# Kernel tuning notes

Hardware: AMD Instinct MI355X
Metric: run time of the kernel (lower is better)

## Reference

```python
import jax, jax.numpy as jnp
import numpy as np

NUM_USER = 24000
NUM_ITEM = 8000
DIM_E = 64
V_DIM = 2048
T_DIM = 384
TOPK = 10
N_UI_LAYERS = 2
LAMBDA = 0.9
N_INTER = 400000


def _build_sim(x):
    xn = x / jnp.linalg.norm(x, axis=-1, keepdims=True)
    return xn @ xn.T


def _knn_sym(sim, topk):
    # top-k per row -> sparse graph with symmetric (D^-1/2 A D^-1/2) normalization
    n = sim.shape[0]
    val, ind = jax.lax.top_k(sim, topk)            # [n, k]
    row = jnp.repeat(jnp.arange(n), topk)
    w = val.reshape(-1)
    col = ind.reshape(-1)
    deg = jax.ops.segment_sum(w, row, num_segments=n)
    dis = jnp.where(deg > 0, deg ** -0.5, 0.0)     # inf -> 0 as in torch masked_fill
    return col, dis[row] * w * dis[col]


def setup_inputs() -> dict:
    key = jax.random.key(0)
    ks = jax.random.split(key, 12)
    user_emb = jax.random.normal(ks[0], (NUM_USER, DIM_E), jnp.float32) * 0.1
    item_emb = jax.random.normal(ks[1], (NUM_ITEM, DIM_E), jnp.float32) * 0.1
    v_feat = jax.random.normal(ks[2], (NUM_ITEM, V_DIM), jnp.float32)
    t_feat = jax.random.normal(ks[3], (NUM_ITEM, T_DIM), jnp.float32)
    W_v = jax.random.normal(ks[4], (V_DIM, DIM_E), jnp.float32) * (1.0 / np.sqrt(V_DIM))
    b_v = jnp.zeros((DIM_E,), jnp.float32)
    W_t = jax.random.normal(ks[5], (T_DIM, DIM_E), jnp.float32) * (1.0 / np.sqrt(T_DIM))
    b_t = jnp.zeros((DIM_E,), jnp.float32)
    Wq1 = jax.random.normal(ks[6], (DIM_E, DIM_E), jnp.float32) * (1.0 / np.sqrt(DIM_E))
    bq1 = jnp.zeros((DIM_E,), jnp.float32)
    wq2 = jax.random.normal(ks[7], (DIM_E,), jnp.float32) * (1.0 / np.sqrt(DIM_E))
    # bipartite user-item interaction edges, symmetrized (as in __init__)
    u = jax.random.randint(ks[8], (N_INTER,), 0, NUM_USER)
    it = jax.random.randint(ks[9], (N_INTER,), 0, NUM_ITEM) + NUM_USER
    ei = jnp.stack([u, it])
    edge_index = jnp.concatenate([ei, ei[::-1]], axis=1)  # [2, 2*N_INTER]
    # original (frozen) multimodal KNN graphs built from raw features at init
    orig_img_cols, orig_img_w = _knn_sym(_build_sim(v_feat), TOPK)
    orig_txt_cols, orig_txt_w = _knn_sym(_build_sim(t_feat), TOPK)
    return {"user_emb": user_emb, "item_emb": item_emb, "v_feat": v_feat,
            "t_feat": t_feat, "W_v": W_v, "b_v": b_v, "W_t": W_t, "b_t": b_t,
            "Wq1": Wq1, "bq1": bq1, "wq2": wq2,
            "orig_img_w": orig_img_w, "orig_txt_w": orig_txt_w,
            "edge_index": edge_index,
            "orig_img_cols": orig_img_cols, "orig_txt_cols": orig_txt_cols}


def reference(user_emb, item_emb, v_feat, t_feat, W_v, b_v, W_t, b_t,
              Wq1, bq1, wq2, orig_img_w, orig_txt_w,
              edge_index, orig_img_cols, orig_txt_cols):
    n_user, n_item = user_emb.shape[0], item_emb.shape[0]
    # modality projections
    image_feats = v_feat @ W_v + b_v
    text_feats = t_feat @ W_t + b_t
    # fresh KNN graphs from projected features (build_item_graph=True path)
    img_cols, img_w = _knn_sym(_build_sim(image_feats), TOPK)
    txt_cols, txt_w = _knn_sym(_build_sim(text_feats), TOPK)
    row = jnp.repeat(jnp.arange(n_item), TOPK)

    def fused_spmm(cols_new, w_new, cols_orig, w_orig, x):
        # (1-lam)*A_new + lam*A_orig, applied as a single sparse matmul
        rows = jnp.concatenate([row, row])
        cols = jnp.concatenate([cols_new, cols_orig])
        w = jnp.concatenate([(1.0 - LAMBDA) * w_new,
                             LAMBDA * jax.lax.stop_gradient(w_orig)])
        return jax.ops.segment_sum(w[:, None] * x[cols], rows, num_segments=n_item)

    # NOTE: source bug reproduced - mm_layers loop always re-reads item_embedding,
    # so effective propagation depth is 1 regardless of mm_layers.
    image_item = fused_spmm(img_cols, img_w, orig_img_cols, orig_img_w, item_emb)
    text_item = fused_spmm(txt_cols, txt_w, orig_txt_cols, orig_txt_w, item_emb)

    def q(x):
        return jnp.tanh(x @ Wq1 + bq1) @ wq2  # [n_item]

    att = jnp.stack([q(image_item), q(text_item)], axis=-1)  # [n_item, 2]
    wgt = jax.nn.softmax(att, axis=-1)
    h = wgt[:, :1] * image_item + wgt[:, 1:] * text_item

    # user-item GCN propagation with sym degree normalization
    ego = jnp.concatenate([user_emb, item_emb], axis=0)
    n = ego.shape[0]
    r, c = edge_index[0], edge_index[1]
    deg = jax.ops.segment_sum(jnp.ones_like(r, dtype=ego.dtype), r, num_segments=n)
    dis = jnp.where(deg > 0, deg ** -0.5, 0.0)
    norm = dis[r] * dis[c]
    embs = [ego]
    for _ in range(N_UI_LAYERS):
        ego = jax.ops.segment_sum(norm[:, None] * ego[c], r, num_segments=n)
        embs.append(ego)
    all_emb = jnp.mean(jnp.stack(embs, axis=1), axis=1)
    u_g, i_g = all_emb[:n_user], all_emb[n_user:]
    h_norm = h / jnp.maximum(jnp.linalg.norm(h, axis=1, keepdims=True), 1e-12)
    i_g = i_g + h_norm
    return jnp.concatenate([u_g, i_g], axis=0)
```

## Files before the change

kernel.cpp:

```cpp
#include <hip/hip_runtime.h>
#include <math.h>

#define N_USER 24000
#define N_ITEM 8000
#define N_NODE 32000
#define N_EDGE 800000
#define NJC    16
#define JCH    512

typedef __attribute__((ext_vector_type(8))) short bf16x8;
typedef __attribute__((ext_vector_type(4))) float f32x4;

__device__ __forceinline__ float wred_sum(float v) {
#pragma unroll
  for (int off = 32; off; off >>= 1) v += __shfl_xor(v, off, 64);
  return v;
}

__device__ __forceinline__ unsigned short f2bf(float f) {
  unsigned int u = __float_as_uint(f);
  unsigned int r = (u + 0x7fffu + ((u >> 16) & 1u)) >> 16;
  return (unsigned short)r;
}
__device__ __forceinline__ float bf2f(unsigned short h) {
  return __uint_as_float(((unsigned int)h) << 16);
}

__device__ __forceinline__ unsigned int umx(unsigned int a, unsigned int b) { return a > b ? a : b; }
__device__ __forceinline__ unsigned int umn(unsigned int a, unsigned int b) { return a < b ? a : b; }

__device__ __forceinline__ float key_val(unsigned int k) {
  return ((float)(int)(k >> 13) - 131080.0f) * (1.0f / 131072.0f);
}
__device__ __forceinline__ int key_idx(unsigned int k) {
  return 8191 - (int)(k & 8191u);
}

__global__ __launch_bounds__(256) void gemm_dual(
    const float* __restrict__ Xi, const float* __restrict__ Wi,
    const float* __restrict__ Xt, const float* __restrict__ Wt,
    float* __restrict__ Pi, float* __restrict__ Pt)
{
  __shared__ float As[32 * 64];
  __shared__ float Bs[32 * 64];
  const int tid = threadIdx.x;
  const int m0 = blockIdx.x * 64;
  const int cy = blockIdx.y;
  const float* X; const float* W; float* out; int K, kc0, Klen;
  if (cy < 8) { X = Xi; W = Wi; K = 2048; Klen = 256; kc0 = cy * 256;
                out = Pi + (size_t)cy * N_ITEM * 64; }
  else        { X = Xt; W = Wt; K = 384;  Klen = 128; kc0 = (cy - 8) * 128;
                out = Pt + (size_t)(cy - 8) * N_ITEM * 64; }
  const int tr = tid >> 4, tc = tid & 15;
  float acc[4][4] = {};
  for (int k0 = kc0; k0 < kc0 + Klen; k0 += 32) {
    __syncthreads();
#pragma unroll
    for (int l = 0; l < 2; ++l) {
      int f4 = tid + l * 256;
      int r = f4 >> 3, kq = f4 & 7;
      float4 a = *(const float4*)(X + (size_t)(m0 + r) * K + k0 + kq * 4);
      As[(kq * 4 + 0) * 64 + r] = a.x;
      As[(kq * 4 + 1) * 64 + r] = a.y;
      As[(kq * 4 + 2) * 64 + r] = a.z;
      As[(kq * 4 + 3) * 64 + r] = a.w;
      int kb = f4 >> 4, nq = f4 & 15;
      *(float4*)(Bs + kb * 64 + nq * 4) =
          *(const float4*)(W + (size_t)(k0 + kb) * 64 + nq * 4);
    }
    __syncthreads();
#pragma unroll
    for (int k = 0; k < 32; ++k) {
      float4 a4 = *(const float4*)(As + k * 64 + tr * 4);
      float4 b4 = *(const float4*)(Bs + k * 64 + tc * 4);
      float av[4] = {a4.x, a4.y, a4.z, a4.w};
      float bv[4] = {b4.x, b4.y, b4.z, b4.w};
#pragma unroll
      for (int ri = 0; ri < 4; ++ri)
#pragma unroll
        for (int ci = 0; ci < 4; ++ci) acc[ri][ci] += av[ri] * bv[ci];
    }
  }
#pragma unroll
  for (int ri = 0; ri < 4; ++ri) {
    float4 o;
    o.x = acc[ri][0]; o.y = acc[ri][1]; o.z = acc[ri][2]; o.w = acc[ri][3];
    *(float4*)(out + (size_t)(m0 + tr * 4 + ri) * 64 + tc * 4) = o;
  }
}

__global__ __launch_bounds__(256) void norm_dual(
    const float* __restrict__ Pi, const float* __restrict__ bi,
    unsigned short* __restrict__ Xhi, unsigned short* __restrict__ Xli,
    const float* __restrict__ Pt, const float* __restrict__ bt,
    unsigned short* __restrict__ Xht, unsigned short* __restrict__ Xlt)
{
  const float* P; const float* bias; unsigned short *Xh, *Xl; int nk;
  if (blockIdx.y == 0) { P = Pi; bias = bi; Xh = Xhi; Xl = Xli; nk = 8; }
  else                 { P = Pt; bias = bt; Xh = Xht; Xl = Xlt; nk = 3; }
  int row = blockIdx.x * 4 + (threadIdx.x >> 6);
  int lane = threadIdx.x & 63;
  size_t o = (size_t)row * 64 + lane;
  float v = bias[lane];
  for (int q = 0; q < nk; ++q) v += P[(size_t)q * N_ITEM * 64 + o];
  float ss = wred_sum(v * v);
  float xn = v * rsqrtf(ss);
  unsigned short hi = f2bf(xn);
  Xh[o] = hi;
  Xl[o] = f2bf(xn - bf2f(hi));
}

__global__ __launch_bounds__(256) void sim_topk_mfma(
    const unsigned short* __restrict__ Xhi, const unsigned short* __restrict__ Xli,
    const unsigned short* __restrict__ Xht, const unsigned short* __restrict__ Xlt,
    unsigned int* __restrict__ pk)
{
  __shared__ char lds[2 * 2 * 32 * 128];
  const unsigned short* Xh = blockIdx.z ? Xht : Xhi;
  const unsigned short* Xl = blockIdx.z ? Xlt : Xli;
  unsigned int* pkm = pk + (size_t)blockIdx.z * N_ITEM * (NJC * 10);

  const int tid = threadIdx.x;
  const int l = tid & 63;
  const int wid = tid >> 6;
  const int ib = blockIdx.x * 128 + wid * 32;
  const int jc = blockIdx.y * JCH;

  bf16x8 bh[2][2], bl[2][2];
#pragma unroll
  for (int s = 0; s < 2; ++s) {
    int irow = ib + s * 16 + (l & 15);
    if (irow > N_ITEM - 1) irow = N_ITEM - 1;
    int ksl = (l >> 4) * 8;
#pragma unroll
    for (int kh = 0; kh < 2; ++kh) {
      bh[s][kh] = *(const bf16x8*)(Xh + (size_t)irow * 64 + kh * 32 + ksl);
      bl[s][kh] = *(const bf16x8*)(Xl + (size_t)irow * 64 + kh * 32 + ksl);
    }
  }

  unsigned int K0[10], K1[10];
#pragma unroll
  for (int t = 0; t < 10; ++t) { K0[t] = 0u; K1[t] = 0u; }

  auto stage = [&](int b, int p) {
    int row = tid >> 3, cb = (tid & 7) * 16;
    int gr = jc + p * 32 + row;
    if (gr > N_ITEM - 1) gr = N_ITEM - 1;
    int4 vh = *(const int4*)(Xh + (size_t)gr * 64 + (cb >> 1));
    int4 vl = *(const int4*)(Xl + (size_t)gr * 64 + (cb >> 1));
    int bo = (row * 128 + cb) ^ ((row & 7) << 4);
    *(int4*)(lds + b * 8192 + bo) = vh;
    *(int4*)(lds + b * 8192 + 4096 + bo) = vl;
  };

  stage(0, 0);
  int cur = 0;
  for (int p = 0; p < 16; ++p) {
    __syncthreads();
    if (p < 15) stage(cur ^ 1, p + 1);
    const char* ldsH = lds + cur * 8192;
    const char* ldsL = ldsH + 4096;
    f32x4 acc[2][2] = {};
#pragma unroll
    for (int t = 0; t < 2; ++t) {
      int jr = t * 16 + (l & 15);
      int sw = (jr & 7) << 4;
      int rb = jr * 128 + ((l >> 4) << 4);
      bf16x8 ah0 = *(const bf16x8*)(ldsH + (rb ^ sw));
      bf16x8 ah1 = *(const bf16x8*)(ldsH + ((rb + 64) ^ sw));
      bf16x8 al0 = *(const bf16x8*)(ldsL + (rb ^ sw));
      bf16x8 al1 = *(const bf16x8*)(ldsL + ((rb + 64) ^ sw));
#pragma unroll
      for (int s = 0; s < 2; ++s) {
        acc[t][s] = __builtin_amdgcn_mfma_f32_16x16x32_bf16(ah0, bh[s][0], acc[t][s], 0, 0, 0);
        acc[t][s] = __builtin_amdgcn_mfma_f32_16x16x32_bf16(ah1, bh[s][1], acc[t][s], 0, 0, 0);
        acc[t][s] = __builtin_amdgcn_mfma_f32_16x16x32_bf16(ah0, bl[s][0], acc[t][s], 0, 0, 0);
        acc[t][s] = __builtin_amdgcn_mfma_f32_16x16x32_bf16(ah1, bl[s][1], acc[t][s], 0, 0, 0);
        acc[t][s] = __builtin_amdgcn_mfma_f32_16x16x32_bf16(al0, bh[s][0], acc[t][s], 0, 0, 0);
        acc[t][s] = __builtin_amdgcn_mfma_f32_16x16x32_bf16(al1, bh[s][1], acc[t][s], 0, 0, 0);
      }
    }
    const int jg0 = jc + p * 32 + ((l >> 4) << 2);
#pragma unroll
    for (int s = 0; s < 2; ++s) {
      unsigned int* K = s ? K1 : K0;
#pragma unroll
      for (int t = 0; t < 2; ++t) {
#pragma unroll
        for (int r = 0; r < 4; ++r) {
          int jj = jg0 + t * 16 + r;
          float f = acc[t][s][r];
          unsigned int v19 = (unsigned int)(int)(f * 131072.0f + 131080.0f);
          unsigned int key = (v19 << 13) | (unsigned int)(8191 - jj);
          key = (jj < N_ITEM) ? key : 0u;
#pragma unroll
          for (int q = 0; q < 10; ++q) {
            unsigned int mn = umn(K[q], key);
            K[q] = umx(K[q], key);
            key = mn;
          }
        }
      }
    }
    cur ^= 1;
  }

#pragma unroll
  for (int s = 0; s < 2; ++s) {
    unsigned int* K = s ? K1 : K0;
    unsigned int kv[10];
#pragma unroll
    for (int t = 0; t < 10; ++t) {
      unsigned int m = K[0];
      m = umx(m, (unsigned int)__shfl_xor((int)m, 16, 64));
      m = umx(m, (unsigned int)__shfl_xor((int)m, 32, 64));
      bool own = (K[0] == m);
#pragma unroll
      for (int q2 = 0; q2 < 9; ++q2) K[q2] = own ? K[q2 + 1] : K[q2];
      K[9] = own ? 0u : K[9];
      kv[t] = m;
    }
    int i = ib + s * 16 + (l & 15);
    if (l < 16 && i < N_ITEM) {
      size_t base = ((size_t)i * NJC + blockIdx.y) * 10;
#pragma unroll
      for (int t = 0; t < 10; ++t) pkm[base + t] = kv[t];
    }
  }
}

__global__ __launch_bounds__(256) void merge_topk(
    const unsigned int* __restrict__ pk,
    float* __restrict__ tv_i, int* __restrict__ tc_i, float* __restrict__ dis_i,
    float* __restrict__ tv_t, int* __restrict__ tc_t, float* __restrict__ dis_t)
{
  float* tv; int* tc; float* dis;
  if (blockIdx.y == 0) { tv = tv_i; tc = tc_i; dis = dis_i; }
  else                 { tv = tv_t; tc = tc_t; dis = dis_t; }
  int lane = threadIdx.x & 63;
  int row = blockIdx.x * 4 + (threadIdx.x >> 6);
  size_t base = (size_t)blockIdx.y * N_ITEM * (NJC * 10) + (size_t)row * (NJC * 10);
  unsigned int k0 = pk[base + lane];
  unsigned int k1 = pk[base + 64 + lane];
  unsigned int k2 = (lane < 32) ? pk[base + 128 + lane] : 0u;
  float deg = 0.f, keepv = 0.f; int keepc = 0;
  for (int t = 0; t < 10; ++t) {
    unsigned int m = umx(umx(k0, k1), k2);
#pragma unroll
    for (int off = 32; off; off >>= 1)
      m = umx(m, (unsigned int)__shfl_xor((int)m, off, 64));
    deg += key_val(m);
    if (k0 == m) k0 = 0u;
    else if (k1 == m) k1 = 0u;
    else if (k2 == m) k2 = 0u;
    if (lane == t) { keepv = key_val(m); keepc = key_idx(m); }
  }
  if (lane < 10) { tv[(size_t)row * 10 + lane] = keepv; tc[(size_t)row * 10 + lane] = keepc; }
  if (lane == 0) dis[row] = deg > 0.f ? rsqrtf(deg) : 0.f;
}

__global__ __launch_bounds__(256) void spmm_attn(
    const float* __restrict__ tv_i, const int* __restrict__ tc_i, const float* __restrict__ dis_i,
    const float* __restrict__ ow_i, const int* __restrict__ oc_i,
    const float* __restrict__ tv_t, const int* __restrict__ tc_t, const float* __restrict__ dis_t,
    const float* __restrict__ ow_t, const int* __restrict__ oc_t,
    const float* __restrict__ item_emb,
    const float* __restrict__ Wq1, const float* __restrict__ bq1,
    const float* __restrict__ wq2, float* __restrict__ hn)
{
  __shared__ float Wlds[64 * 64];
  __shared__ float sm[4][2][64];
  int tid = threadIdx.x;
  int lane = tid & 63, wid = tid >> 6;
  int row = blockIdx.x * 4 + wid;
#pragma unroll
  for (int s = 0; s < 4; ++s) {
    int idx = tid + s * 256;
    ((float4*)Wlds)[idx] = ((const float4*)Wq1)[idx];
  }
  float a0 = 0.f, a1 = 0.f;
  {
    float disr = dis_i[row];
#pragma unroll
    for (int t = 0; t < 10; ++t) {
      int c = tc_i[(size_t)row * 10 + t];
      a0 += 0.1f * disr * tv_i[(size_t)row * 10 + t] * dis_i[c] * item_emb[(size_t)c * 64 + lane];
    }
#pragma unroll
    for (int t = 0; t < 10; ++t) {
      int c = oc_i[(size_t)row * 10 + t];
      a0 += 0.9f * ow_i[(size_t)row * 10 + t] * item_emb[(size_t)c * 64 + lane];
    }
  }
  {
    float disr = dis_t[row];
#pragma unroll
    for (int t = 0; t < 10; ++t) {
      int c = tc_t[(size_t)row * 10 + t];
      a1 += 0.1f * disr * tv_t[(size_t)row * 10 + t] * dis_t[c] * item_emb[(size_t)c * 64 + lane];
    }
#pragma unroll
    for (int t = 0; t < 10; ++t) {
      int c = oc_t[(size_t)row * 10 + t];
      a1 += 0.9f * ow_t[(size_t)row * 10 + t] * item_emb[(size_t)c * 64 + lane];
    }
  }
  sm[wid][0][lane] = a0;
  sm[wid][1][lane] = a1;
  __syncthreads();
  float y0 = bq1[lane], y1 = bq1[lane];
  for (int k = 0; k < 64; ++k) {
    float w = Wlds[k * 64 + lane];
    y0 += sm[wid][0][k] * w;
    y1 += sm[wid][1][k] * w;
  }
  float wq = wq2[lane];
  float s0 = wred_sum(tanhf(y0) * wq);
  float s1 = wred_sum(tanhf(y1) * wq);
  float mx = fmaxf(s0, s1);
  float e0 = expf(s0 - mx), e1 = expf(s1 - mx);
  float inv = 1.f / (e0 + e1);
  float h = (e0 * inv) * a0 + (e1 * inv) * a1;
  float n2 = wred_sum(h * h);
  float nrm = fmaxf(sqrtf(n2), 1e-12f);
  hn[(size_t)row * 64 + lane] = h / nrm;
}

__global__ void ui_zero(int* degi, int* cursor)
{
  int n = blockIdx.x * 256 + threadIdx.x;
  if (n < N_NODE) { degi[n] = 0; cursor[n] = 0; }
}

__global__ void ui_count(const int* __restrict__ r, int* degi)
{
  int e = blockIdx.x * 256 + threadIdx.x;
  if (e < N_EDGE) atomicAdd(&degi[r[e]], 1);
}

__global__ __launch_bounds__(256) void ui_blocksum(const int* __restrict__ degi, int* __restrict__ bsum)
{
  __shared__ int ws4[4];
  int tid = threadIdx.x;
  int v = degi[blockIdx.x * 256 + tid];
#pragma unroll
  for (int off = 32; off; off >>= 1) v += __shfl_xor(v, off, 64);
  if ((tid & 63) == 0) ws4[tid >> 6] = v;
  __syncthreads();
  if (tid == 0) bsum[blockIdx.x] = ws4[0] + ws4[1] + ws4[2] + ws4[3];
}

__global__ __launch_bounds__(128) void ui_scanb(const int* __restrict__ bsum, int* __restrict__ bbase, int* __restrict__ offs)
{
  __shared__ int s[128];
  int t = threadIdx.x;
  int v = (t < 125) ? bsum[t] : 0;
  s[t] = v;
  __syncthreads();
  for (int off = 1; off < 128; off <<= 1) {
    int tmp = (t >= off) ? s[t - off] : 0;
    __syncthreads();
    s[t] += tmp;
    __syncthreads();
  }
  if (t < 125) bbase[t] = s[t] - v;
  if (t == 127) offs[N_NODE] = s[127];
}

__global__ __launch_bounds__(256) void ui_scanc(const int* __restrict__ degi, const int* __restrict__ bbase,
                                                int* __restrict__ offs, float* __restrict__ disui)
{
  __shared__ int wt[4];
  int tid = threadIdx.x;
  int i = blockIdx.x * 256 + tid;
  int d = degi[i];
  int v = d;
#pragma unroll
  for (int off = 1; off < 64; off <<= 1) {
    int n = __shfl_up(v, off, 64);
    if ((tid & 63) >= off) v += n;
  }
  if ((tid & 63) == 63) wt[tid >> 6] = v;
  __syncthreads();
  int add = bbase[blockIdx.x];
  for (int w = 0; w < (tid >> 6); ++w) add += wt[w];
  offs[i] = add + v - d;
  disui[i] = d > 0 ? rsqrtf((float)d) : 0.f;
}

__global__ void ui_fill(const int* __restrict__ r, const int* __restrict__ c,
                        const int* __restrict__ offs, int* cursor, int* __restrict__ csr)
{
  int e = blockIdx.x * 256 + threadIdx.x;
  if (e < N_EDGE) {
    int rr = r[e];
    int pos = offs[rr] + atomicAdd(&cursor[rr], 1);
    csr[pos] = c[e];
  }
}

template <bool FIRST, bool FINAL>
__global__ __launch_bounds__(256) void ui_prop(
    const float* __restrict__ in, const float* __restrict__ ue,
    const float* __restrict__ ie, float* __restrict__ out,
    const int* __restrict__ offs, const int* __restrict__ csr,
    const float* __restrict__ dis, const float* __restrict__ hn)
{
  int tid = threadIdx.x;
  int lane = tid & 63, wid = tid >> 6;
  int row = blockIdx.x * 4 + wid;
  int q = lane >> 4, c4 = lane & 15;
  float4 acc = make_float4(0.f, 0.f, 0.f, 0.f);
  int e0 = offs[row], e1 = offs[row + 1];
  for (int e = e0 + q; e < e1; e += 4) {
    int cc = csr[e];
    const float* src = FIRST
        ? (cc < N_USER ? ue + (size_t)cc * 64 : ie + (size_t)(cc - N_USER) * 64)
        : in + (size_t)cc * 64;
    float4 v = *(const float4*)(src + c4 * 4);
    float d = dis[cc];
    acc.x += d * v.x; acc.y += d * v.y; acc.z += d * v.z; acc.w += d * v.w;
  }
#pragma unroll
  for (int off = 16; off <= 32; off <<= 1) {
    acc.x += __shfl_xor(acc.x, off, 64);
    acc.y += __shfl_xor(acc.y, off, 64);
    acc.z += __shfl_xor(acc.z, off, 64);
    acc.w += __shfl_xor(acc.w, off, 64);
  }
  if (q == 0) {
    float dr = dis[row];
    acc.x *= dr; acc.y *= dr; acc.z *= dr; acc.w *= dr;
    if (!FINAL) {
      *(float4*)(out + (size_t)row * 64 + c4 * 4) = acc;
    } else {
      float4 ego = (row < N_USER)
          ? *(const float4*)(ue + (size_t)row * 64 + c4 * 4)
          : *(const float4*)(ie + (size_t)(row - N_USER) * 64 + c4 * 4);
      float4 l1 = *(const float4*)(in + (size_t)row * 64 + c4 * 4);
      float4 o;
      o.x = (ego.x + l1.x + acc.x) * (1.f / 3.f);
      o.y = (ego.y + l1.y + acc.y) * (1.f / 3.f);
      o.z = (ego.z + l1.z + acc.z) * (1.f / 3.f);
      o.w = (ego.w + l1.w + acc.w) * (1.f / 3.f);
      if (row >= N_USER) {
        float4 h = *(const float4*)(hn + (size_t)(row - N_USER) * 64 + c4 * 4);
        o.x += h.x; o.y += h.y; o.z += h.z; o.w += h.w;
      }
      *(float4*)(out + (size_t)row * 64 + c4 * 4) = o;
    }
  }
}

extern "C" void kernel_launch(void* const* d_in, const int* in_sizes, int n_in,
                              void* d_out, int out_size, void* d_ws, size_t ws_size,
                              hipStream_t stream)
{
  (void)in_sizes; (void)n_in; (void)out_size; (void)ws_size;
  const float* user_emb = (const float*)d_in[0];
  const float* item_emb = (const float*)d_in[1];
  const float* v_feat   = (const float*)d_in[2];
  const float* t_feat   = (const float*)d_in[3];
  const float* W_v      = (const float*)d_in[4];
  const float* b_v      = (const float*)d_in[5];
  const float* W_t      = (const float*)d_in[6];
  const float* b_t      = (const float*)d_in[7];
  const float* Wq1      = (const float*)d_in[8];
  const float* bq1      = (const float*)d_in[9];
  const float* wq2      = (const float*)d_in[10];
  const float* ow_i     = (const float*)d_in[11];
  const float* ow_t     = (const float*)d_in[12];
  const int*   eidx     = (const int*)d_in[13];
  const int*   oc_i     = (const int*)d_in[14];
  const int*   oc_t     = (const int*)d_in[15];
  float* out = (float*)d_out;

  char* wp = (char*)d_ws;
  auto alloc = [&](size_t bytes) -> void* {
    void* p = (void*)wp;
    wp += (bytes + 255) & ~(size_t)255;
    return p;
  };
  char* regionA = (char*)alloc((size_t)8 * N_ITEM * 64 * 4 + 1024);
  char* regionB = (char*)alloc((size_t)N_NODE * 64 * 4 + 1024);
  float* Pp_i = (float*)regionA;
  float* Pp_t = (float*)regionB;
  unsigned int* pk = (unsigned int*)regionA;
  float* E1 = (float*)regionB;

  unsigned short* Xhi = (unsigned short*)alloc((size_t)N_ITEM * 64 * 2);
  unsigned short* Xli = (unsigned short*)alloc((size_t)N_ITEM * 64 * 2);
  unsigned short* Xht = (unsigned short*)alloc((size_t)N_ITEM * 64 * 2);
  unsigned short* Xlt = (unsigned short*)alloc((size_t)N_ITEM * 64 * 2);
  float* tv_i  = (float*)alloc((size_t)N_ITEM * 10 * 4);
  int*   tc_i  = (int*)  alloc((size_t)N_ITEM * 10 * 4);
  float* dis_i = (float*)alloc((size_t)N_ITEM * 4);
  float* tv_t  = (float*)alloc((size_t)N_ITEM * 10 * 4);
  int*   tc_t  = (int*)  alloc((size_t)N_ITEM * 10 * 4);
  float* dis_t = (float*)alloc((size_t)N_ITEM * 4);
  float* hn    = (float*)alloc((size_t)N_ITEM * 64 * 4);
  int*   degi  = (int*)  alloc((size_t)N_NODE * 4);
  int*   curs  = (int*)  alloc((size_t)N_NODE * 4);
  int*   offs  = (int*)  alloc((size_t)(N_NODE + 1) * 4);
  float* disui = (float*)alloc((size_t)N_NODE * 4);
  int*   csr   = (int*)  alloc((size_t)N_EDGE * 4);
  int*   bsum  = (int*)  alloc((size_t)128 * 4);
  int*   bbase = (int*)  alloc((size_t)128 * 4);

  gemm_dual<<<dim3(125, 11), 256, 0, stream>>>(v_feat, W_v, t_feat, W_t, Pp_i, Pp_t);
  norm_dual<<<dim3(2000, 2), 256, 0, stream>>>(Pp_i, b_v, Xhi, Xli, Pp_t, b_t, Xht, Xlt);
  sim_topk_mfma<<<dim3(63, NJC, 2), 256, 0, stream>>>(Xhi, Xli, Xht, Xlt, pk);
  merge_topk<<<dim3(2000, 2), 256, 0, stream>>>(pk, tv_i, tc_i, dis_i, tv_t, tc_t, dis_t);
  spmm_attn<<<2000, 256, 0, stream>>>(tv_i, tc_i, dis_i, ow_i, oc_i,
                                      tv_t, tc_t, dis_t, ow_t, oc_t,
                                      item_emb, Wq1, bq1, wq2, hn);
  ui_zero<<<125, 256, 0, stream>>>(degi, curs);
  ui_count<<<N_EDGE / 256, 256, 0, stream>>>(eidx, degi);
  ui_blocksum<<<125, 256, 0, stream>>>(degi, bsum);
  ui_scanb<<<1, 128, 0, stream>>>(bsum, bbase, offs);
  ui_scanc<<<125, 256, 0, stream>>>(degi, bbase, offs, disui);
  ui_fill<<<N_EDGE / 256, 256, 0, stream>>>(eidx, eidx + N_EDGE, offs, curs, csr);
  ui_prop<true, false><<<8000, 256, 0, stream>>>(nullptr, user_emb, item_emb, E1, offs, csr, disui, nullptr);
  ui_prop<false, true><<<8000, 256, 0, stream>>>(E1, user_emb, item_emb, out, offs, csr, disui, hn);
}
```

Before: 320.0 us.

## Enlarge GEMM row tile, specialize top-k epilogue masking, widen SpMM lanes

The projection GEMM now computes a 128-row tile per block, giving each thread 8x4 outputs, and pads the A tile stride in LDS. This halves the block count and clamps out-of-range rows. The similarity top-k epilogue precomputes the inverted column indices and applies the out-of-range mask only in the last column chunk. The UI propagation kernel has each lane handle 8 floats per edge and processes 8 edges in parallel per row, with one extra shuffle stage. These are separate local tweaks meant to raise arithmetic intensity and cut per-element overhead, at the cost of higher register use and fewer GEMM blocks.

```diff
diff --git a/kernel.cpp b/kernel.cpp
--- a/kernel.cpp
+++ b/kernel.cpp
@@ -36,15 +36,16 @@
   return 8191 - (int)(k & 8191u);
 }
 
+#define ASTR 132
 __global__ __launch_bounds__(256) void gemm_dual(
     const float* __restrict__ Xi, const float* __restrict__ Wi,
     const float* __restrict__ Xt, const float* __restrict__ Wt,
     float* __restrict__ Pi, float* __restrict__ Pt)
 {
-  __shared__ float As[32 * 64];
+  __shared__ float As[32 * ASTR];
   __shared__ float Bs[32 * 64];
   const int tid = threadIdx.x;
-  const int m0 = blockIdx.x * 64;
+  const int m0 = blockIdx.x * 128;
   const int cy = blockIdx.y;
   const float* X; const float* W; float* out; int K, kc0, Klen;
   if (cy < 8) { X = Xi; W = Wi; K = 2048; Klen = 256; kc0 = cy * 256;
@@ -52,40 +53,49 @@
   else        { X = Xt; W = Wt; K = 384;  Klen = 128; kc0 = (cy - 8) * 128;
                 out = Pt + (size_t)(cy - 8) * N_ITEM * 64; }
   const int tr = tid >> 4, tc = tid & 15;
-  float acc[4][4] = {};
+  float acc[8][4] = {};
   for (int k0 = kc0; k0 < kc0 + Klen; k0 += 32) {
     __syncthreads();
 #pragma unroll
-    for (int l = 0; l < 2; ++l) {
-      int f4 = tid + l * 256;
-      int r = f4 >> 3, kq = f4 & 7;
-      float4 a = *(const float4*)(X + (size_t)(m0 + r) * K + k0 + kq * 4);
-      As[(kq * 4 + 0) * 64 + r] = a.x;
-      As[(kq * 4 + 1) * 64 + r] = a.y;
-      As[(kq * 4 + 2) * 64 + r] = a.z;
-      As[(kq * 4 + 3) * 64 + r] = a.w;
-      int kb = f4 >> 4, nq = f4 & 15;
+    for (int lq = 0; lq < 4; ++lq) {
+      int u = tid + lq * 256;
+      int r = u >> 3, kq = u & 7;
+      int row = m0 + r; if (row > N_ITEM - 1) row = N_ITEM - 1;
+      float4 a = *(const float4*)(X + (size_t)row * K + k0 + kq * 4);
+      As[(kq * 4 + 0) * ASTR + r] = a.x;
+      As[(kq * 4 + 1) * ASTR + r] = a.y;
+      As[(kq * 4 + 2) * ASTR + r] = a.z;
+      As[(kq * 4 + 3) * ASTR + r] = a.w;
+    }
+#pragma unroll
+    for (int lq = 0; lq < 2; ++lq) {
+      int u = tid + lq * 256;
+      int kb = u >> 4, nq = u & 15;
       *(float4*)(Bs + kb * 64 + nq * 4) =
           *(const float4*)(W + (size_t)(k0 + kb) * 64 + nq * 4);
     }
     __syncthreads();
 #pragma unroll
     for (int k = 0; k < 32; ++k) {
-      float4 a4 = *(const float4*)(As + k * 64 + tr * 4);
+      float4 a0 = *(const float4*)(As + k * ASTR + tr * 8);
+      float4 a1 = *(const float4*)(As + k * ASTR + tr * 8 + 4);
       float4 b4 = *(const float4*)(Bs + k * 64 + tc * 4);
-      float av[4] = {a4.x, a4.y, a4.z, a4.w};
+      float av[8] = {a0.x, a0.y, a0.z, a0.w, a1.x, a1.y, a1.z, a1.w};
       float bv[4] = {b4.x, b4.y, b4.z, b4.w};
 #pragma unroll
-      for (int ri = 0; ri < 4; ++ri)
+      for (int ri = 0; ri < 8; ++ri)
 #pragma unroll
         for (int ci = 0; ci < 4; ++ci) acc[ri][ci] += av[ri] * bv[ci];
     }
   }
 #pragma unroll
-  for (int ri = 0; ri < 4; ++ri) {
-    float4 o;
-    o.x = acc[ri][0]; o.y = acc[ri][1]; o.z = acc[ri][2]; o.w = acc[ri][3];
-    *(float4*)(out + (size_t)(m0 + tr * 4 + ri) * 64 + tc * 4) = o;
+  for (int ri = 0; ri < 8; ++ri) {
+    int row = m0 + tr * 8 + ri;
+    if (row < N_ITEM) {
+      float4 o;
+      o.x = acc[ri][0]; o.y = acc[ri][1]; o.z = acc[ri][2]; o.w = acc[ri][3];
+      *(float4*)(out + (size_t)row * 64 + tc * 4) = o;
+    }
   }
 }
 
@@ -125,6 +135,7 @@
   const int wid = tid >> 6;
   const int ib = blockIdx.x * 128 + wid * 32;
   const int jc = blockIdx.y * JCH;
+  const bool lastc = (jc + JCH > N_ITEM);
 
   bf16x8 bh[2][2], bl[2][2];
 #pragma unroll
@@ -154,6 +165,28 @@
     *(int4*)(lds + b * 8192 + 4096 + bo) = vl;
   };
 
+#define EPI(MASKED)                                                            \
+  _Pragma("unroll")                                                            \
+  for (int s = 0; s < 2; ++s) {                                                \
+    unsigned int* K = s ? K1 : K0;                                             \
+    _Pragma("unroll")                                                          \
+    for (int t = 0; t < 2; ++t) {                                              \
+      _Pragma("unroll")                                                        \
+      for (int r = 0; r < 4; ++r) {                                            \
+        float f = acc[t][s][r];                                                \
+        unsigned int v19 = (unsigned int)(int)(f * 131072.0f + 131080.0f);     \
+        unsigned int key = (v19 << 13) | (unsigned int)jinv[t * 4 + r];        \
+        if (MASKED) key = (jinv[t * 4 + r] >= 192) ? key : 0u;                 \
+        _Pragma("unroll")                                                      \
+        for (int q = 0; q < 10; ++q) {                                         \
+          unsigned int mn = umn(K[q], key);                                    \
+          K[q] = umx(K[q], key);                                               \
+          key = mn;                                                            \
+        }                                                                      \
+      }                                                                        \
+    }                                                                          \
+  }
+
   stage(0, 0);
   int cur = 0;
   for (int p = 0; p < 16; ++p) {
@@ -182,29 +215,16 @@
       }
     }
     const int jg0 = jc + p * 32 + ((l >> 4) << 2);
-#pragma unroll
-    for (int s = 0; s < 2; ++s) {
-      unsigned int* K = s ? K1 : K0;
-#pragma unroll
-      for (int t = 0; t < 2; ++t) {
-#pragma unroll
-        for (int r = 0; r < 4; ++r) {
-          int jj = jg0 + t * 16 + r;
-          float f = acc[t][s][r];
-          unsigned int v19 = (unsigned int)(int)(f * 131072.0f + 131080.0f);
-          unsigned int key = (v19 << 13) | (unsigned int)(8191 - jj);
-          key = (jj < N_ITEM) ? key : 0u;
-#pragma unroll
-          for (int q = 0; q < 10; ++q) {
-            unsigned int mn = umn(K[q], key);
-            K[q] = umx(K[q], key);
-            key = mn;
-          }
-        }
-      }
-    }
+    int jinv[8];
+#pragma unroll
+    for (int t = 0; t < 2; ++t)
+#pragma unroll
+      for (int r = 0; r < 4; ++r)
+        jinv[t * 4 + r] = 8191 - (jg0 + t * 16 + r);
+    if (!lastc) { EPI(false) } else { EPI(true) }
     cur ^= 1;
   }
+#undef EPI
 
 #pragma unroll
   for (int s = 0; s < 2; ++s) {
@@ -410,45 +430,64 @@
   int tid = threadIdx.x;
   int lane = tid & 63, wid = tid >> 6;
   int row = blockIdx.x * 4 + wid;
-  int q = lane >> 4, c4 = lane & 15;
-  float4 acc = make_float4(0.f, 0.f, 0.f, 0.f);
+  int q = lane >> 3, c8 = lane & 7;
+  float4 acc0 = make_float4(0.f, 0.f, 0.f, 0.f);
+  float4 acc1 = make_float4(0.f, 0.f, 0.f, 0.f);
   int e0 = offs[row], e1 = offs[row + 1];
-  for (int e = e0 + q; e < e1; e += 4) {
+  for (int e = e0 + q; e < e1; e += 8) {
     int cc = csr[e];
     const float* src = FIRST
         ? (cc < N_USER ? ue + (size_t)cc * 64 : ie + (size_t)(cc - N_USER) * 64)
         : in + (size_t)cc * 64;
-    float4 v = *(const float4*)(src + c4 * 4);
+    float4 v0 = *(const float4*)(src + c8 * 8);
+    float4 v1 = *(const float4*)(src + c8 * 8 + 4);
     float d = dis[cc];
-    acc.x += d * v.x; acc.y += d * v.y; acc.z += d * v.z; acc.w += d * v.w;
-  }
-#pragma unroll
-  for (int off = 16; off <= 32; off <<= 1) {
-    acc.x += __shfl_xor(acc.x, off, 64);
-    acc.y += __shfl_xor(acc.y, off, 64);
-    acc.z += __shfl_xor(acc.z, off, 64);
-    acc.w += __shfl_xor(acc.w, off, 64);
+    acc0.x += d * v0.x; acc0.y += d * v0.y; acc0.z += d * v0.z; acc0.w += d * v0.w;
+    acc1.x += d * v1.x; acc1.y += d * v1.y; acc1.z += d * v1.z; acc1.w += d * v1.w;
+  }
+#pragma unroll
+  for (int off = 8; off <= 32; off <<= 1) {
+    acc0.x += __shfl_xor(acc0.x, off, 64);
+    acc0.y += __shfl_xor(acc0.y, off, 64);
+    acc0.z += __shfl_xor(acc0.z, off, 64);
+    acc0.w += __shfl_xor(acc0.w, off, 64);
+    acc1.x += __shfl_xor(acc1.x, off, 64);
+    acc1.y += __shfl_xor(acc1.y, off, 64);
+    acc1.z += __shfl_xor(acc1.z, off, 64);
+    acc1.w += __shfl_xor(acc1.w, off, 64);
   }
   if (q == 0) {
     float dr = dis[row];
-    acc.x *= dr; acc.y *= dr; acc.z *= dr; acc.w *= dr;
+    acc0.x *= dr; acc0.y *= dr; acc0.z *= dr; acc0.w *= dr;
+    acc1.x *= dr; acc1.y *= dr; acc1.z *= dr; acc1.w *= dr;
     if (!FINAL) {
-      *(float4*)(out + (size_t)row * 64 + c4 * 4) = acc;
+      *(float4*)(out + (size_t)row * 64 + c8 * 8) = acc0;
+      *(float4*)(out + (size_t)row * 64 + c8 * 8 + 4) = acc1;
     } else {
-      float4 ego = (row < N_USER)
-          ? *(const float4*)(ue + (size_t)row * 64 + c4 * 4)
-          : *(const float4*)(ie + (size_t)(row - N_USER) * 64 + c4 * 4);
-      float4 l1 = *(const float4*)(in + (size_t)row * 64 + c4 * 4);
-      float4 o;
-      o.x = (ego.x + l1.x + acc.x) * (1.f / 3.f);
-      o.y = (ego.y + l1.y + acc.y) * (1.f / 3.f);
-      o.z = (ego.z + l1.z + acc.z) * (1.f / 3.f);
-      o.w = (ego.w + l1.w + acc.w) * (1.f / 3.f);
+      const float* egop = (row < N_USER) ? ue + (size_t)row * 64
+                                         : ie + (size_t)(row - N_USER) * 64;
+      float4 eg0 = *(const float4*)(egop + c8 * 8);
+      float4 eg1 = *(const float4*)(egop + c8 * 8 + 4);
+      float4 l10 = *(const float4*)(in + (size_t)row * 64 + c8 * 8);
+      float4 l11 = *(const float4*)(in + (size_t)row * 64 + c8 * 8 + 4);
+      float4 o0, o1;
+      o0.x = (eg0.x + l10.x + acc0.x) * (1.f / 3.f);
+      o0.y = (eg0.y + l10.y + acc0.y) * (1.f / 3.f);
+      o0.z = (eg0.z + l10.z + acc0.z) * (1.f / 3.f);
+      o0.w = (eg0.w + l10.w + acc0.w) * (1.f / 3.f);
+      o1.x = (eg1.x + l11.x + acc1.x) * (1.f / 3.f);
+      o1.y = (eg1.y + l11.y + acc1.y) * (1.f / 3.f);
+      o1.z = (eg1.z + l11.z + acc1.z) * (1.f / 3.f);
+      o1.w = (eg1.w + l11.w + acc1.w) * (1.f / 3.f);
       if (row >= N_USER) {
-        float4 h = *(const float4*)(hn + (size_t)(row - N_USER) * 64 + c4 * 4);
-        o.x += h.x; o.y += h.y; o.z += h.z; o.w += h.w;
+        const float* hp = hn + (size_t)(row - N_USER) * 64;
+        float4 h0 = *(const float4*)(hp + c8 * 8);
+        float4 h1 = *(const float4*)(hp + c8 * 8 + 4);
+        o0.x += h0.x; o0.y += h0.y; o0.z += h0.z; o0.w += h0.w;
+        o1.x += h1.x; o1.y += h1.y; o1.z += h1.z; o1.w += h1.w;
       }
-      *(float4*)(out + (size_t)row * 64 + c4 * 4) = o;
+      *(float4*)(out + (size_t)row * 64 + c8 * 8) = o0;
+      *(float4*)(out + (size_t)row * 64 + c8 * 8 + 4) = o1;
     }
   }
 }
@@ -508,7 +547,7 @@
   int*   bsum  = (int*)  alloc((size_t)128 * 4);
   int*   bbase = (int*)  alloc((size_t)128 * 4);
 
-  gemm_dual<<<dim3(125, 11), 256, 0, stream>>>(v_feat, W_v, t_feat, W_t, Pp_i, Pp_t);
+  gemm_dual<<<dim3(63, 11), 256, 0, stream>>>(v_feat, W_v, t_feat, W_t, Pp_i, Pp_t);
   norm_dual<<<dim3(2000, 2), 256, 0, stream>>>(Pp_i, b_v, Xhi, Xli, Pp_t, b_t, Xht, Xlt);
   sim_topk_mfma<<<dim3(63, NJC, 2), 256, 0, stream>>>(Xhi, Xli, Xht, Xlt, pk);
   merge_topk<<<dim3(2000, 2), 256, 0, stream>>>(pk, tv_i, tc_i, dis_i, tv_t, tc_t, dis_t);
```

Result: faster. 308.3 us (-3.7%).
